# Kernel tuning notes

Measured on AMD Instinct MI355X. Metric: run time of the kernel, lower is better.

## Reference

```python
import jax, jax.numpy as jnp
import numpy as np

N_ATOMS = 8_388_608
N_MOL = 65_536
FIDELITY_LEVEL = 1
FIDELITY_OFFSET = 200
SAE_SIZE = 518  # (fidelity_level+1)*offset + 118


def setup_inputs() -> dict:
    key = jax.random.key(0)
    k1, k2, k3, k4 = jax.random.split(key, 4)
    numbers = jax.random.randint(k1, (N_ATOMS,), 0, 119, dtype=jnp.int32)
    mol_idx = jnp.sort(jax.random.randint(k2, (N_ATOMS,), 0, N_MOL, dtype=jnp.int32))
    energy = jax.random.normal(k3, (N_MOL,), dtype=jnp.float32)
    sae_tensor = jax.random.normal(k4, (SAE_SIZE,), dtype=jnp.float32)
    return {"energy": energy, "sae_tensor": sae_tensor, "numbers": numbers, "mol_idx": mol_idx}


def reference(energy, sae_tensor, numbers, mol_idx):
    # embedding-style gather: per-atom SAE energy at shifted atomic number
    shifted = numbers + FIDELITY_LEVEL * FIDELITY_OFFSET
    sae_per_atom = sae_tensor[shifted]  # [N_ATOMS]
    # per-molecule segment sum (replaces the Python loop over molecules)
    sae_energy = jax.ops.segment_sum(sae_per_atom, mol_idx, num_segments=N_MOL)  # [N_MOL]
    return energy + sae_energy
```

## Files before the change

### kernel.cpp

```cpp
#include <hip/hip_runtime.h>


#define SAE_WINDOW 119
#define SAE_SHIFT  200

__global__ __launch_bounds__(256)
void sae_segsum_kernel(const float* __restrict__ sae,
                       const int*   __restrict__ numbers,
                       const int*   __restrict__ mol_idx,
                       float*       __restrict__ out,
                       int n_vec4, int stride)
{
    __shared__ float s_sae[128];
    const int tid  = threadIdx.x;
    if (tid < SAE_WINDOW) s_sae[tid] = sae[SAE_SHIFT + tid];
    __syncthreads();

    const int lane = tid & 63;
    const int gtid = blockIdx.x * blockDim.x + tid;

    const int4* __restrict__ num4 = (const int4*)numbers;
    const int4* __restrict__ mol4 = (const int4*)mol_idx;

    const int iters = (n_vec4 + stride - 1) / stride;

    for (int it = 0; it < iters; ++it) {
        const int i = gtid + it * stride;
        int   key = -1;
        float val = 0.0f;

        if (i < n_vec4) {
            const int4 n = num4[i];
            const int4 m = mol4[i];
            const float v0 = s_sae[n.x];
            const float v1 = s_sae[n.y];
            const float v2 = s_sae[n.z];
            const float v3 = s_sae[n.w];

            int cur = m.x; float acc = v0;
            if (m.y == cur) acc += v1; else { atomicAdd(&out[cur], acc); cur = m.y; acc = v1; }
            if (m.z == cur) acc += v2; else { atomicAdd(&out[cur], acc); cur = m.z; acc = v2; }
            if (m.w == cur) acc += v3; else { atomicAdd(&out[cur], acc); cur = m.w; acc = v3; }
            key = cur; val = acc;
        }

        #pragma unroll
        for (int d = 1; d < 64; d <<= 1) {
            const int   okey = __shfl_down(key, d, 64);
            const float oval = __shfl_down(val, d, 64);
            if ((lane + d) < 64 && okey == key) val += oval;
        }
        const int pkey = __shfl_up(key, 1, 64);
        if (key >= 0 && (lane == 0 || pkey != key)) {
            atomicAdd(&out[key], val);
        }
    }
}

__global__ void sae_tail_kernel(const float* __restrict__ sae,
                                const int*   __restrict__ numbers,
                                const int*   __restrict__ mol_idx,
                                float*       __restrict__ out,
                                int start, int n_atoms)
{
    int i = start + blockIdx.x * blockDim.x + threadIdx.x;
    if (i < n_atoms) {
        atomicAdd(&out[mol_idx[i]], sae[numbers[i] + SAE_SHIFT]);
    }
}

extern "C" void kernel_launch(void* const* d_in, const int* in_sizes, int n_in,
                              void* d_out, int out_size, void* d_ws, size_t ws_size,
                              hipStream_t stream) {
    const float* energy  = (const float*)d_in[0];
    const float* sae     = (const float*)d_in[1];
    const int*   numbers = (const int*)d_in[2];
    const int*   mol_idx = (const int*)d_in[3];
    float*       out     = (float*)d_out;

    const int n_atoms = in_sizes[2];
    const int n_vec4  = n_atoms >> 2;

    hipMemcpyAsync(out, energy, (size_t)out_size * sizeof(float),
                   hipMemcpyDeviceToDevice, stream);

    const int block  = 256;
    const int grid   = 2048;
    const int stride = grid * block;

    sae_segsum_kernel<<<grid, block, 0, stream>>>(sae, numbers, mol_idx, out,
                                                  n_vec4, stride);

    const int rem = n_atoms & 3;
    if (rem) {
        sae_tail_kernel<<<1, 64, 0, stream>>>(sae, numbers, mol_idx, out,
                                              n_vec4 << 2, n_atoms);
    }
}
```

Measured before the change: 102.2 us.

## Process 16 atoms per thread with nontemporal loads and one-shot grid

Adds a specialized kernel for atom counts divisible by 4096 where each thread loads four contiguous int4 vectors of numbers and molecule indices with nontemporal loads, merges 16 atoms serially, then does one wavefront segmented reduction. This replaces the grid-stride loop, cutting shuffle-reduction and atomic traffic per atom by a factor of four and giving more loads in flight per thread. The trade-off is higher register pressure, a strided per-thread access pattern across the four vectors, and an added dispatch branch.

```diff
diff --git a/kernel.cpp b/kernel.cpp
--- a/kernel.cpp
+++ b/kernel.cpp
@@ -4,56 +4,96 @@
 #define SAE_WINDOW 119
 #define SAE_SHIFT  200
 
+typedef int iv4 __attribute__((ext_vector_type(4)));
+
+__device__ __forceinline__ iv4 ntload(const iv4* p) {
+    return __builtin_nontemporal_load(p);
+}
+
+#define MERGE_ATOM(KEY, NUM)                                            \
+    {                                                                   \
+        const float v = s_sae[(NUM)];                                   \
+        if ((KEY) == cur) acc += v;                                     \
+        else { atomicAdd(&out[cur], acc); cur = (KEY); acc = v; }       \
+    }
+
+__device__ __forceinline__ void epilogue(int key, float val,
+                                         float* __restrict__ out,
+                                         const int lane)
+{
+    #pragma unroll
+    for (int d = 1; d < 64; d <<= 1) {
+        const int   okey = __shfl_down(key, d, 64);
+        const float oval = __shfl_down(val, d, 64);
+        if ((lane + d) < 64 && okey == key) val += oval;
+    }
+    const int pkey = __shfl_up(key, 1, 64);
+    if (key >= 0 && (lane == 0 || pkey != key)) {
+        atomicAdd(&out[key], val);
+    }
+}
+
 __global__ __launch_bounds__(256)
-void sae_segsum_kernel(const float* __restrict__ sae,
-                       const int*   __restrict__ numbers,
-                       const int*   __restrict__ mol_idx,
-                       float*       __restrict__ out,
-                       int n_vec4, int stride)
+void sae_segsum_16(const float* __restrict__ sae,
+                   const iv4*   __restrict__ num4,
+                   const iv4*   __restrict__ mol4,
+                   float*       __restrict__ out)
 {
     __shared__ float s_sae[128];
-    const int tid  = threadIdx.x;
+    const int tid = threadIdx.x;
     if (tid < SAE_WINDOW) s_sae[tid] = sae[SAE_SHIFT + tid];
     __syncthreads();
 
     const int lane = tid & 63;
-    const int gtid = blockIdx.x * blockDim.x + tid;
+    const int base = (blockIdx.x * 256 + tid) * 4;
 
-    const int4* __restrict__ num4 = (const int4*)numbers;
-    const int4* __restrict__ mol4 = (const int4*)mol_idx;
+    const iv4 n0 = ntload(&num4[base + 0]);
+    const iv4 n1 = ntload(&num4[base + 1]);
+    const iv4 n2 = ntload(&num4[base + 2]);
+    const iv4 n3 = ntload(&num4[base + 3]);
+    const iv4 m0 = ntload(&mol4[base + 0]);
+    const iv4 m1 = ntload(&mol4[base + 1]);
+    const iv4 m2 = ntload(&mol4[base + 2]);
+    const iv4 m3 = ntload(&mol4[base + 3]);
 
+    int   cur = m0.x;
+    float acc = s_sae[n0.x];
+    MERGE_ATOM(m0.y, n0.y) MERGE_ATOM(m0.z, n0.z) MERGE_ATOM(m0.w, n0.w)
+    MERGE_ATOM(m1.x, n1.x) MERGE_ATOM(m1.y, n1.y) MERGE_ATOM(m1.z, n1.z) MERGE_ATOM(m1.w, n1.w)
+    MERGE_ATOM(m2.x, n2.x) MERGE_ATOM(m2.y, n2.y) MERGE_ATOM(m2.z, n2.z) MERGE_ATOM(m2.w, n2.w)
+    MERGE_ATOM(m3.x, n3.x) MERGE_ATOM(m3.y, n3.y) MERGE_ATOM(m3.z, n3.z) MERGE_ATOM(m3.w, n3.w)
+
+    epilogue(cur, acc, out, lane);
+}
+
+__global__ __launch_bounds__(256)
+void sae_segsum_generic(const float* __restrict__ sae,
+                        const iv4*   __restrict__ num4,
+                        const iv4*   __restrict__ mol4,
+                        float*       __restrict__ out,
+                        int n_vec4, int stride)
+{
+    __shared__ float s_sae[128];
+    const int tid = threadIdx.x;
+    if (tid < SAE_WINDOW) s_sae[tid] = sae[SAE_SHIFT + tid];
+    __syncthreads();
+
+    const int lane = tid & 63;
     const int iters = (n_vec4 + stride - 1) / stride;
 
     for (int it = 0; it < iters; ++it) {
-        const int i = gtid + it * stride;
+        const int i = blockIdx.x * blockDim.x + tid + it * stride;
         int   key = -1;
         float val = 0.0f;
-
         if (i < n_vec4) {
-            const int4 n = num4[i];
-            const int4 m = mol4[i];
-            const float v0 = s_sae[n.x];
-            const float v1 = s_sae[n.y];
-            const float v2 = s_sae[n.z];
-            const float v3 = s_sae[n.w];
-
-            int cur = m.x; float acc = v0;
-            if (m.y == cur) acc += v1; else { atomicAdd(&out[cur], acc); cur = m.y; acc = v1; }
-            if (m.z == cur) acc += v2; else { atomicAdd(&out[cur], acc); cur = m.z; acc = v2; }
-            if (m.w == cur) acc += v3; else { atomicAdd(&out[cur], acc); cur = m.w; acc = v3; }
+            const iv4 n = num4[i];
+            const iv4 m = mol4[i];
+            int   cur = m.x;
+            float acc = s_sae[n.x];
+            MERGE_ATOM(m.y, n.y) MERGE_ATOM(m.z, n.z) MERGE_ATOM(m.w, n.w)
             key = cur; val = acc;
         }
-
-        #pragma unroll
-        for (int d = 1; d < 64; d <<= 1) {
-            const int   okey = __shfl_down(key, d, 64);
-            const float oval = __shfl_down(val, d, 64);
-            if ((lane + d) < 64 && okey == key) val += oval;
-        }
-        const int pkey = __shfl_up(key, 1, 64);
-        if (key >= 0 && (lane == 0 || pkey != key)) {
-            atomicAdd(&out[key], val);
-        }
+        epilogue(key, val, out, lane);
     }
 }
 
@@ -84,12 +124,20 @@
     hipMemcpyAsync(out, energy, (size_t)out_size * sizeof(float),
                    hipMemcpyDeviceToDevice, stream);
 
-    const int block  = 256;
-    const int grid   = 2048;
-    const int stride = grid * block;
+    const iv4* num4 = (const iv4*)numbers;
+    const iv4* mol4 = (const iv4*)mol_idx;
 
-    sae_segsum_kernel<<<grid, block, 0, stream>>>(sae, numbers, mol_idx, out,
-                                                  n_vec4, stride);
+    const int block = 256;
+
+    if ((n_atoms & 4095) == 0 && n_atoms == (n_atoms / 4096) * 4096) {
+        const int grid = n_atoms / (block * 16);
+        sae_segsum_16<<<grid, block, 0, stream>>>(sae, num4, mol4, out);
+    } else {
+        const int grid   = 2048;
+        const int stride = grid * block;
+        sae_segsum_generic<<<grid, block, 0, stream>>>(sae, num4, mol4, out,
+                                                       n_vec4, stride);
+    }
 
     const int rem = n_atoms & 3;
     if (rem) {
```

Result: slower. 116.4 us (+13.9%).
